# Optimization experiments

Measured on AMD Instinct MI355X. Metric: run time of the kernel, lower is better.

The kernel has to match this reference:

```python
import math
import jax, jax.numpy as jnp
import numpy as np

PROB_SPARSE_FACTOR = 0.4


def setup_inputs() -> dict:
    key = jax.random.key(0)
    kq, kk, kv = jax.random.split(key, 3)
    B, H, T, S, D = 2, 16, 2048, 2048, 64
    q = jax.random.normal(kq, (B, H, T, D), dtype=jnp.float32)
    k = jax.random.normal(kk, (B, H, S, D), dtype=jnp.float32)
    v = jax.random.normal(kv, (B, H, S, D), dtype=jnp.float32)
    return {"q": q, "k": k, "v": v}


def reference(q, k, v):
    B, H, T, D = q.shape
    S = k.shape[2]
    scaling = 1.0 / math.sqrt(D)
    # Informer-style top-u query count (static, derived from shapes)
    u = max(int(min(PROB_SPARSE_FACTOR * math.log(S), T * 0.5)), int(T * 0.3))

    # KLD scoring over full attention approximation: [B,H,T,S]
    attn_approx = jnp.einsum("bhtd,bhsd->bhts", q * scaling, k)
    attn_approx = jnp.clip(attn_approx, -50.0, 50.0)
    attn_approx = attn_approx - jnp.max(attn_approx, axis=-1, keepdims=True)
    sm = jax.nn.softmax(attn_approx, axis=-1)
    log_uniform = math.log(S)
    kl_score = jnp.sum(sm * (jnp.log(sm + 1e-10) + log_uniform), axis=-1)  # [B,H,T]

    # Select top-u most informative queries per (b,h)
    _, topk_idx = jax.lax.top_k(kl_score, u)  # [B,H,u]

    # Sparse attention only for selected queries
    q_red = jnp.take_along_axis(q, topk_idx[..., None], axis=2)  # [B,H,u,D]
    scores = jnp.einsum("bhud,bhsd->bhus", q_red, k) * scaling
    scores = jnp.clip(scores, -50.0, 50.0)
    scores = scores - jnp.max(scores, axis=-1, keepdims=True)
    w = jax.nn.softmax(scores, axis=-1)
    w = jnp.clip(w, 1e-9, 1.0)
    out_red = jnp.einsum("bhus,bhsd->bhud", w, v)  # [B,H,u,D]

    # Scatter reduced outputs back into a zero-initialized full output
    b_i = jnp.arange(B)[:, None, None]
    h_i = jnp.arange(H)[None, :, None]
    out = jnp.zeros_like(q).at[b_i, h_i, topk_idx].set(out_red)
    return out
```

## Files before the change

kernel.cpp:

```cpp
#include <hip/hip_runtime.h>
#include <math.h>

#define T_DIM 2048
#define S_DIM 2048
#define D_DIM 64
#define BH_DIM 32
#define U_SEL 614
#define QROWS 32
#define LOG_S_D 7.624618986159398
#define LOG2E_F 1.4426950408889634f
#define LN2_D 0.6931471805599453
#define SCL_Q (0.125f * LOG2E_F)

typedef __attribute__((ext_vector_type(8))) short bf16x8;
typedef __attribute__((ext_vector_type(4))) short bf16x4;
typedef __attribute__((ext_vector_type(4))) float f32x4;

__device__ __forceinline__ unsigned short bf16_rne(float x) {
  unsigned u = __float_as_uint(x);
  u += 0x7FFF + ((u >> 16) & 1);
  return (unsigned short)(u >> 16);
}
__device__ __forceinline__ float bf16_to_f(unsigned short h) {
  return __uint_as_float(((unsigned)h) << 16);
}
#if defined(__has_builtin)
#if __has_builtin(__builtin_amdgcn_exp2f)
#define EXP2_HW(x) __builtin_amdgcn_exp2f(x)
#endif
#endif
#ifndef EXP2_HW
#define EXP2_HW(x) exp2f(x)
#endif

#define GLD_LDS16(g, l)                                                        \
  __builtin_amdgcn_global_load_lds(                                            \
      (const __attribute__((address_space(1))) unsigned int*)(const void*)(g), \
      (__attribute__((address_space(3))) unsigned int*)(void*)(l), 16, 0, 0)

__device__ __forceinline__ void stage_img16(const unsigned short* __restrict__ g,
                                            unsigned short* l, int lane, int w) {
#pragma unroll
  for (int it = 0; it < 4; ++it) {
    const int chunk = it * 4 + w;
    GLD_LDS16((const char*)g + chunk * 1024 + lane * 16, (char*)l + chunk * 1024);
  }
}
__device__ __forceinline__ void stage_img8(const unsigned short* __restrict__ g,
                                           unsigned short* l, int lane, int w) {
#pragma unroll
  for (int it = 0; it < 2; ++it) {
    const int chunk = it * 4 + w;
    GLD_LDS16((const char*)g + chunk * 1024 + lane * 16, (char*)l + chunk * 1024);
  }
}

__device__ __forceinline__ bf16x8 ldfrag_sw(const unsigned short* buf, int row, int chunk) {
  return *(const bf16x8*)(buf + (row << 6) + (((chunk) ^ (row & 7)) << 3));
}
__device__ __forceinline__ bf16x8 ldfrag_k128(const unsigned short* buf, int row, int chunk) {
  return *(const bf16x8*)(buf + ((row >> 6) << 12) + ((row & 63) << 6) +
                          (((chunk) ^ (row & 7)) << 3));
}

__global__ __launch_bounds__(256) void convert_kernel(
    const float* __restrict__ kin, const float* __restrict__ vin,
    const float* __restrict__ qin, unsigned short* __restrict__ kimg,
    unsigned short* __restrict__ vt_g, unsigned short* __restrict__ qimg,
    float* __restrict__ out) {
  __shared__ float vld[128][65];
  const int jb = blockIdx.x;
  const int tid = threadIdx.x;
  if (jb < 2048) {
    const bool isq = jb >= 1024;
    const int jj = jb & 1023;
    const int bh = jj >> 5, tl = jj & 31;
    const float* src = (isq ? qin : kin) + ((size_t)bh * 2048 + tl * 64) * 64;
    unsigned short* dst = (isq ? qimg : kimg) + (size_t)(bh * 32 + tl) * 8192;
    const float scl = isq ? SCL_Q : 1.0f;
#pragma unroll
    for (int g = 0; g < 2; ++g) {
      const int flat = g * 256 + tid;
      const int r = flat >> 3, c = flat & 7;
      const float4 f0 = *(const float4*)(src + r * 64 + c * 8);
      const float4 f1 = *(const float4*)(src + r * 64 + c * 8 + 4);
      const float xs[8] = {f0.x, f0.y, f0.z, f0.w, f1.x, f1.y, f1.z, f1.w};
      bf16x8 hv, lv;
#pragma unroll
      for (int j = 0; j < 8; ++j) {
        const float x = xs[j] * scl;
        const unsigned short h = bf16_rne(x);
        hv[j] = (short)h;
        lv[j] = (short)bf16_rne(x - bf16_to_f(h));
      }
      const int base = (r << 6) + ((c ^ (r & 7)) << 3);
      *(bf16x8*)(dst + base) = hv;
      *(bf16x8*)(dst + 4096 + base) = lv;
    }
  } else if (jb < 2560) {
    const int jv = jb - 2048;
    const int bh = jv >> 4, tl = jv & 15;
    const float* src = vin + ((size_t)bh * 2048 + tl * 128) * 64;
#pragma unroll
    for (int g = 0; g < 8; ++g) {
      const int f = g * 256 + tid;
      const int r = f >> 4, c4 = f & 15;
      const float4 x = *(const float4*)(src + r * 64 + c4 * 4);
      vld[r][c4 * 4 + 0] = x.x;
      vld[r][c4 * 4 + 1] = x.y;
      vld[r][c4 * 4 + 2] = x.z;
      vld[r][c4 * 4 + 3] = x.w;
    }
    __syncthreads();
    unsigned short* dst = vt_g + (size_t)(bh * 16 + tl) * 8192;
#pragma unroll
    for (int g = 0; g < 4; ++g) {
      const int oc = g * 256 + tid;
      const int w4 = oc >> 8, dt = (oc >> 6) & 3, qd = (oc >> 4) & 3, l = oc & 15;
      bf16x8 hv;
#pragma unroll
      for (int j = 0; j < 8; ++j)
        hv[j] = (short)bf16_rne(vld[w4 * 32 + qd * 8 + j][dt * 16 + l]);
      *(bf16x8*)(dst + oc * 8) = hv;
    }
  } else {
    float4* o4 = (float4*)out;
    const size_t b = (size_t)(jb - 2560);
#pragma unroll
    for (int g = 0; g < 8; ++g)
      o4[b * 2048 + g * 256 + tid] = make_float4(0.f, 0.f, 0.f, 0.f);
  }
}

__global__ __launch_bounds__(256, 2) void kl_score_mfma(
    const unsigned short* __restrict__ qimg, const unsigned short* __restrict__ kimg,
    float2* __restrict__ zw) {
  __shared__ __align__(16) unsigned short lbuf[2][8192];
  const int b = blockIdx.x;
  const int bh = b & 31;
  const int tt = (b >> 5) & 15;
  const int shalf = b >> 9;
  const int tid = threadIdx.x;
  const int lane = tid & 63, w = tid >> 6, quad = lane >> 4, l15 = lane & 15;
  const unsigned short* qb = qimg + (size_t)(bh * 32 + tt * 2) * 8192;
  const unsigned short* kb = kimg + (size_t)bh * (32 * 8192);
  const int tg0 = shalf * 16;

  stage_img16(qb, &lbuf[0][0], lane, w);
  stage_img16(qb + 8192, &lbuf[1][0], lane, w);
  __syncthreads();

  bf16x8 ah[2][2], al[2][2];
#pragma unroll
  for (int rt = 0; rt < 2; ++rt) {
    const int row = w * 32 + rt * 16 + l15;
    const unsigned short* lb = &lbuf[row >> 6][0];
    const int r64 = row & 63;
#pragma unroll
    for (int kc = 0; kc < 2; ++kc) {
      const int off = (r64 << 6) + (((kc * 4 + quad) ^ (r64 & 7)) << 3);
      ah[rt][kc] = *(const bf16x8*)(lb + off);
      al[rt][kc] = *(const bf16x8*)(lb + 4096 + off);
    }
  }
  __syncthreads();

  stage_img16(kb + (size_t)tg0 * 8192, &lbuf[0][0], lane, w);
  __syncthreads();

  float Zf[8], Wf[8];
#pragma unroll
  for (int i = 0; i < 8; ++i) { Zf[i] = 0.f; Wf[i] = 0.f; }

  for (int t = 0; t < 16; ++t) {
    if (t < 15)
      stage_img16(kb + (size_t)(tg0 + t + 1) * 8192, &lbuf[(t + 1) & 1][0], lane, w);
    const unsigned short* cb = &lbuf[t & 1][0];

    f32x4 acc[2][4];
#pragma unroll
    for (int rt = 0; rt < 2; ++rt)
#pragma unroll
      for (int ct = 0; ct < 4; ++ct) acc[rt][ct] = (f32x4){0.f, 0.f, 0.f, 0.f};

#pragma unroll
    for (int ct = 0; ct < 4; ++ct) {
      const int srow = ct * 16 + l15;
      const bf16x8 bh0 = ldfrag_sw(cb, srow, quad);
      const bf16x8 bl0 = ldfrag_sw(cb + 4096, srow, quad);
      const bf16x8 bh1 = ldfrag_sw(cb, srow, 4 + quad);
      const bf16x8 bl1 = ldfrag_sw(cb + 4096, srow, 4 + quad);
#pragma unroll
      for (int rt = 0; rt < 2; ++rt) {
        f32x4 c = acc[rt][ct];
        c = __builtin_amdgcn_mfma_f32_16x16x32_bf16(ah[rt][0], bh0, c, 0, 0, 0);
        c = __builtin_amdgcn_mfma_f32_16x16x32_bf16(al[rt][0], bh0, c, 0, 0, 0);
        c = __builtin_amdgcn_mfma_f32_16x16x32_bf16(ah[rt][0], bl0, c, 0, 0, 0);
        c = __builtin_amdgcn_mfma_f32_16x16x32_bf16(ah[rt][1], bh1, c, 0, 0, 0);
        c = __builtin_amdgcn_mfma_f32_16x16x32_bf16(al[rt][1], bh1, c, 0, 0, 0);
        c = __builtin_amdgcn_mfma_f32_16x16x32_bf16(ah[rt][1], bl1, c, 0, 0, 0);
        acc[rt][ct] = c;
      }
    }

#pragma unroll
    for (int rt = 0; rt < 2; ++rt)
#pragma unroll
      for (int r = 0; r < 4; ++r) {
        float zp = 0.f, wp = 0.f;
#pragma unroll
        for (int ct = 0; ct < 4; ++ct) {
          const float tv = acc[rt][ct][r];
          const float e = EXP2_HW(tv);
          zp += e;
          wp = fmaf(e, tv, wp);
        }
        Zf[rt * 4 + r] += zp;
        Wf[rt * 4 + r] += wp;
      }
    __syncthreads();
  }

#pragma unroll
  for (int i = 0; i < 8; ++i) {
    float Zt = Zf[i], Wt = Wf[i];
#pragma unroll
    for (int mask = 1; mask <= 8; mask <<= 1) {
      Zt += __shfl_xor(Zt, mask);
      Wt += __shfl_xor(Wt, mask);
    }
    if (l15 == 0) {
      const int row = tt * 128 + w * 32 + (i >> 2) * 16 + quad * 4 + (i & 3);
      zw[((size_t)shalf * 32 + bh) * 2048 + row] = make_float2(Zt, Wt);
    }
  }
}

__global__ __launch_bounds__(1024) void topk_kernel(const float2* __restrict__ zw,
                                                    int* __restrict__ topk) {
  __shared__ float sv[2048];
  __shared__ int si[2048];
  const int bh = blockIdx.x;
  const int tid = threadIdx.x;
  for (int i = tid; i < 2048; i += 1024) {
    const float2 a = zw[(size_t)bh * 2048 + i];
    const float2 c = zw[(size_t)(32 + bh) * 2048 + i];
    const double Z = (double)a.x + (double)c.x;
    const double W = (double)a.y + (double)c.y;
    sv[i] = (float)(LN2_D * (W / Z) - log(Z) + LOG_S_D);
    si[i] = i;
  }
  __syncthreads();
  for (int kk = 2; kk <= 2048; kk <<= 1) {
    for (int j = kk >> 1; j > 0; j >>= 1) {
      const int p = tid;
      const int i = ((p & ~(j - 1)) << 1) | (p & (j - 1));
      const int pr = i | j;
      const float v1 = sv[i], v2 = sv[pr];
      const int i1 = si[i], i2 = si[pr];
      const bool beforePI = (v2 > v1) || (v2 == v1 && i2 < i1);
      const bool dirDesc = ((i & kk) == 0);
      const bool doSwap = dirDesc ? beforePI : !beforePI;
      if (doSwap) { sv[i] = v2; sv[pr] = v1; si[i] = i2; si[pr] = i1; }
      __syncthreads();
    }
  }
  for (int i = tid; i < U_SEL; i += 1024) topk[bh * U_SEL + i] = si[i];
}

struct __align__(16) SmC {
  union {
    unsigned short kt[2][8192];
    struct { float obuf[QROWS * 64]; float zred[4][QROWS]; } o;
  } a;
  union { unsigned short qs[QROWS * 64]; unsigned short ps[4][QROWS * 40]; } c;
};

__global__ __launch_bounds__(256, 3) void sparse_attn_mfma(
    const float* __restrict__ q, const unsigned short* __restrict__ kimg,
    const unsigned short* __restrict__ vt_g, const int* __restrict__ topk,
    float* __restrict__ out) {
  __shared__ SmC sm;
  const int b = blockIdx.x;
  const int bh = b & 31;
  const int l0 = (b >> 5) * QROWS;
  const int tid = threadIdx.x;
  const int lane = tid & 63, w = tid >> 6, quad = lane >> 4, l15 = lane & 15;
  const float* qb = q + (size_t)bh * (2048 * 64);
  const unsigned short* kb = kimg + (size_t)bh * (32 * 8192);
  const unsigned short* vtb = vt_g + (size_t)bh * (16 * 8192);
  const int* tkb = topk + bh * U_SEL;

  {
    const int ch = tid;
    const int r = ch >> 3, c = ch & 7;
    const int l = l0 + r;
    const int row = (l < U_SEL) ? tkb[l] : tkb[0];
    const float4 f0 = *(const float4*)(qb + (size_t)row * 64 + c * 8);
    const float4 f1 = *(const float4*)(qb + (size_t)row * 64 + c * 8 + 4);
    const float xs[8] = {f0.x, f0.y, f0.z, f0.w, f1.x, f1.y, f1.z, f1.w};
    bf16x8 hv;
#pragma unroll
    for (int j = 0; j < 8; ++j) hv[j] = (short)bf16_rne(xs[j] * SCL_Q);
    *(bf16x8*)&sm.c.qs[(r << 6) + ((c ^ (r & 7)) << 3)] = hv;
  }
  stage_img8(kb, sm.a.kt[0], lane, w);
  stage_img8(kb + 8192, sm.a.kt[0] + 4096, lane, w);
  __syncthreads();

  bf16x8 qf[2][2];
#pragma unroll
  for (int nt = 0; nt < 2; ++nt)
#pragma unroll
    for (int kc = 0; kc < 2; ++kc)
      qf[nt][kc] = ldfrag_sw(sm.c.qs, nt * 16 + l15, kc * 4 + quad);
  __syncthreads();

  float zrun[2] = {0.f, 0.f};
  f32x4 oacc[2][4];
#pragma unroll
  for (int a = 0; a < 2; ++a)
#pragma unroll
    for (int b2 = 0; b2 < 4; ++b2) oacc[a][b2] = (f32x4){0.f, 0.f, 0.f, 0.f};

  for (int st = 0; st < 16; ++st) {
    if (st < 15) {
      unsigned short* kd = sm.a.kt[(st + 1) & 1];
      stage_img8(kb + (size_t)(2 * st + 2) * 8192, kd, lane, w);
      stage_img8(kb + (size_t)(2 * st + 3) * 8192, kd + 4096, lane, w);
    }
    const char* vp = (const char*)(vtb + (size_t)st * 8192);
    bf16x8 vbf[4];
#pragma unroll
    for (int dt = 0; dt < 4; ++dt)
      vbf[dt] = *(const bf16x8*)(vp + w * 4096 + dt * 1024 + lane * 16);

    const unsigned short* kcur = sm.a.kt[st & 1];

    const int ar0 = w * 32 + l15, ar1 = w * 32 + 16 + l15;
    const bf16x8 a00 = ldfrag_k128(kcur, ar0, quad);
    const bf16x8 a01 = ldfrag_k128(kcur, ar0, 4 + quad);
    const bf16x8 a10 = ldfrag_k128(kcur, ar1, quad);
    const bf16x8 a11 = ldfrag_k128(kcur, ar1, 4 + quad);

    f32x4 sacc[2][2];
    __builtin_amdgcn_s_setprio(1);
#pragma unroll
    for (int mt = 0; mt < 2; ++mt)
#pragma unroll
      for (int nt = 0; nt < 2; ++nt) {
        f32x4 c = (f32x4){0.f, 0.f, 0.f, 0.f};
        c = __builtin_amdgcn_mfma_f32_16x16x32_bf16(mt ? a10 : a00, qf[nt][0], c, 0, 0, 0);
        c = __builtin_amdgcn_mfma_f32_16x16x32_bf16(mt ? a11 : a01, qf[nt][1], c, 0, 0, 0);
        sacc[mt][nt] = c;
      }
    __builtin_amdgcn_s_setprio(0);

#pragma unroll
    for (int nt = 0; nt < 2; ++nt) {
      float zl = 0.f;
#pragma unroll
      for (int mt = 0; mt < 2; ++mt) {
        bf16x4 pw;
#pragma unroll
        for (int r = 0; r < 4; ++r) {
          const float p = EXP2_HW(sacc[mt][nt][r]);
          zl += p;
          pw[r] = (short)bf16_rne(p);
        }
        *(bf16x4*)&sm.c.ps[w][(nt * 16 + l15) * 40 + mt * 16 + quad * 4] = pw;
      }
      zrun[nt] += zl;
    }

    __builtin_amdgcn_s_setprio(1);
#pragma unroll
    for (int mtq = 0; mtq < 2; ++mtq) {
      const bf16x8 pa = *(const bf16x8*)&sm.c.ps[w][(mtq * 16 + l15) * 40 + quad * 8];
#pragma unroll
      for (int dt = 0; dt < 4; ++dt)
        oacc[mtq][dt] = __builtin_amdgcn_mfma_f32_16x16x32_bf16(pa, vbf[dt], oacc[mtq][dt], 0, 0, 0);
    }
    __builtin_amdgcn_s_setprio(0);
    __syncthreads();
  }

#pragma unroll
  for (int nt = 0; nt < 2; ++nt) {
    float z = zrun[nt];
    z += __shfl_xor(z, 16);
    z += __shfl_xor(z, 32);
    if (quad == 0) sm.a.o.zred[w][nt * 16 + l15] = z;
  }
  for (int i = tid; i < QROWS * 64; i += 256) sm.a.o.obuf[i] = 0.f;
  __syncthreads();
#pragma unroll
  for (int mtq = 0; mtq < 2; ++mtq)
#pragma unroll
    for (int r = 0; r < 4; ++r) {
      const int qr = mtq * 16 + quad * 4 + r;
#pragma unroll
      for (int dt = 0; dt < 4; ++dt)
        atomicAdd(&sm.a.o.obuf[qr * 64 + dt * 16 + l15], oacc[mtq][dt][r]);
    }
  __syncthreads();
  {
    if (tid < QROWS * 4) {
      const int qr = tid >> 2, seg = tid & 3;
      const int l = l0 + qr;
      if (l < U_SEL) {
        const float Zt = sm.a.o.zred[0][qr] + sm.a.o.zred[1][qr] +
                         sm.a.o.zred[2][qr] + sm.a.o.zred[3][qr];
        const float inv = 1.0f / Zt;
        const int row = tkb[l];
        float* op = &out[((size_t)bh * T_DIM + row) * 64 + seg * 16];
        const float* ob = &sm.a.o.obuf[qr * 64 + seg * 16];
#pragma unroll
        for (int j = 0; j < 4; ++j) {
          float4 o;
          o.x = ob[j * 4 + 0] * inv;
          o.y = ob[j * 4 + 1] * inv;
          o.z = ob[j * 4 + 2] * inv;
          o.w = ob[j * 4 + 3] * inv;
          *(float4*)&op[j * 4] = o;
        }
      }
    }
  }
}

extern "C" void kernel_launch(void* const* d_in, const int* in_sizes, int n_in,
                              void* d_out, int out_size, void* d_ws, size_t ws_size,
                              hipStream_t stream) {
  const float* q = (const float*)d_in[0];
  const float* k = (const float*)d_in[1];
  const float* v = (const float*)d_in[2];
  float* out = (float*)d_out;
  char* ws = (char*)d_ws;
  float2* zw = (float2*)ws;
  int* topk = (int*)(ws + 1048576);
  unsigned short* kimg = (unsigned short*)(ws + 1310720);
  unsigned short* vt_g = (unsigned short*)(ws + 18087936);
  unsigned short* qimg = (unsigned short*)(ws + 26476544);

  convert_kernel<<<dim3(3072), dim3(256), 0, stream>>>(k, v, q, kimg, vt_g, qimg, out);
  kl_score_mfma<<<dim3(1024), dim3(256), 0, stream>>>(qimg, kimg, zw);
  topk_kernel<<<dim3(BH_DIM), dim3(1024), 0, stream>>>(zw, topk);
  sparse_attn_mfma<<<dim3(768), dim3(256), 0, stream>>>(q, kimg, vt_g, topk, out);
}
```

Measured before the change: 220.2 us.

## Pre-layout K in MFMA fragment order and load directly to registers

The convert kernel now also writes a third copy of the high bf16 part of K, laid out in MFMA fragment order per wave. The sparse attention kernel loads its A fragments straight from global memory into registers, so the LDS double-buffered K staging and the per-iteration __syncthreads are gone. This lowers LDS use and removes block-wide barriers in the main loop. In exchange the convert kernel does extra global writes, and global load latency is no longer hidden by the asynchronous LDS prefetch.

```diff
diff --git a/kernel.cpp b/kernel.cpp
--- a/kernel.cpp
+++ b/kernel.cpp
@@ -46,14 +46,6 @@
     GLD_LDS16((const char*)g + chunk * 1024 + lane * 16, (char*)l + chunk * 1024);
   }
 }
-__device__ __forceinline__ void stage_img8(const unsigned short* __restrict__ g,
-                                           unsigned short* l, int lane, int w) {
-#pragma unroll
-  for (int it = 0; it < 2; ++it) {
-    const int chunk = it * 4 + w;
-    GLD_LDS16((const char*)g + chunk * 1024 + lane * 16, (char*)l + chunk * 1024);
-  }
-}
 
 __device__ __forceinline__ bf16x8 ldfrag_sw(const unsigned short* buf, int row, int chunk) {
   return *(const bf16x8*)(buf + (row << 6) + (((chunk) ^ (row & 7)) << 3));
@@ -67,7 +59,7 @@
     const float* __restrict__ kin, const float* __restrict__ vin,
     const float* __restrict__ qin, unsigned short* __restrict__ kimg,
     unsigned short* __restrict__ vt_g, unsigned short* __restrict__ qimg,
-    float* __restrict__ out) {
+    unsigned short* __restrict__ kcimg, float* __restrict__ out) {
   __shared__ float vld[128][65];
   const int jb = blockIdx.x;
   const int tid = threadIdx.x;
@@ -77,6 +69,7 @@
     const int bh = jj >> 5, tl = jj & 31;
     const float* src = (isq ? qin : kin) + ((size_t)bh * 2048 + tl * 64) * 64;
     unsigned short* dst = (isq ? qimg : kimg) + (size_t)(bh * 32 + tl) * 8192;
+    unsigned short* kcd = kcimg + (size_t)(bh * 16 + (tl >> 1)) * 8192;
     const float scl = isq ? SCL_Q : 1.0f;
 #pragma unroll
     for (int g = 0; g < 2; ++g) {
@@ -96,6 +89,11 @@
       const int base = (r << 6) + ((c ^ (r & 7)) << 3);
       *(bf16x8*)(dst + base) = hv;
       *(bf16x8*)(dst + 4096 + base) = lv;
+      if (!isq) {
+        const int s_local = ((tl & 1) << 6) + r;
+        const int wv = s_local >> 5, mtk = (r >> 4) & 1, kcc = c >> 2, qdd = c & 3;
+        *(bf16x8*)(kcd + (wv * 4 + mtk * 2 + kcc) * 512 + qdd * 128 + ((r & 15) << 3)) = hv;
+      }
     }
   } else if (jb < 2560) {
     const int jv = jb - 2048;
@@ -269,15 +267,13 @@
 }
 
 struct __align__(16) SmC {
-  union {
-    unsigned short kt[2][8192];
-    struct { float obuf[QROWS * 64]; float zred[4][QROWS]; } o;
-  } a;
   union { unsigned short qs[QROWS * 64]; unsigned short ps[4][QROWS * 40]; } c;
+  float obuf[QROWS * 64];
+  float zred[4][QROWS];
 };
 
 __global__ __launch_bounds__(256, 3) void sparse_attn_mfma(
-    const float* __restrict__ q, const unsigned short* __restrict__ kimg,
+    const float* __restrict__ q, const unsigned short* __restrict__ kcimg,
     const unsigned short* __restrict__ vt_g, const int* __restrict__ topk,
     float* __restrict__ out) {
   __shared__ SmC sm;
@@ -287,13 +283,12 @@
   const int tid = threadIdx.x;
   const int lane = tid & 63, w = tid >> 6, quad = lane >> 4, l15 = lane & 15;
   const float* qb = q + (size_t)bh * (2048 * 64);
-  const unsigned short* kb = kimg + (size_t)bh * (32 * 8192);
-  const unsigned short* vtb = vt_g + (size_t)bh * (16 * 8192);
+  const char* kcb = (const char*)(kcimg + (size_t)bh * (16 * 8192));
+  const char* vtb = (const char*)(vt_g + (size_t)bh * (16 * 8192));
   const int* tkb = topk + bh * U_SEL;
 
   {
-    const int ch = tid;
-    const int r = ch >> 3, c = ch & 7;
+    const int r = tid >> 3, c = tid & 7;
     const int l = l0 + r;
     const int row = (l < U_SEL) ? tkb[l] : tkb[0];
     const float4 f0 = *(const float4*)(qb + (size_t)row * 64 + c * 8);
@@ -304,8 +299,6 @@
     for (int j = 0; j < 8; ++j) hv[j] = (short)bf16_rne(xs[j] * SCL_Q);
     *(bf16x8*)&sm.c.qs[(r << 6) + ((c ^ (r & 7)) << 3)] = hv;
   }
-  stage_img8(kb, sm.a.kt[0], lane, w);
-  stage_img8(kb + 8192, sm.a.kt[0] + 4096, lane, w);
   __syncthreads();
 
   bf16x8 qf[2][2];
@@ -324,24 +317,18 @@
     for (int b2 = 0; b2 < 4; ++b2) oacc[a][b2] = (f32x4){0.f, 0.f, 0.f, 0.f};
 
   for (int st = 0; st < 16; ++st) {
-    if (st < 15) {
-      unsigned short* kd = sm.a.kt[(st + 1) & 1];
-      stage_img8(kb + (size_t)(2 * st + 2) * 8192, kd, lane, w);
-      stage_img8(kb + (size_t)(2 * st + 3) * 8192, kd + 4096, lane, w);
-    }
-    const char* vp = (const char*)(vtb + (size_t)st * 8192);
+    const char* kp = kcb + (size_t)st * 16384;
+    bf16x8 af[2][2];
+#pragma unroll
+    for (int mt = 0; mt < 2; ++mt)
+#pragma unroll
+      for (int kc = 0; kc < 2; ++kc)
+        af[mt][kc] = *(const bf16x8*)(kp + ((w * 4 + mt * 2 + kc) << 10) + lane * 16);
+    const char* vp = vtb + (size_t)st * 16384;
     bf16x8 vbf[4];
 #pragma unroll
     for (int dt = 0; dt < 4; ++dt)
-      vbf[dt] = *(const bf16x8*)(vp + w * 4096 + dt * 1024 + lane * 16);
-
-    const unsigned short* kcur = sm.a.kt[st & 1];
-
-    const int ar0 = w * 32 + l15, ar1 = w * 32 + 16 + l15;
-    const bf16x8 a00 = ldfrag_k128(kcur, ar0, quad);
-    const bf16x8 a01 = ldfrag_k128(kcur, ar0, 4 + quad);
-    const bf16x8 a10 = ldfrag_k128(kcur, ar1, quad);
-    const bf16x8 a11 = ldfrag_k128(kcur, ar1, 4 + quad);
+      vbf[dt] = *(const bf16x8*)(vp + ((w * 4 + dt) << 10) + lane * 16);
 
     f32x4 sacc[2][2];
     __builtin_amdgcn_s_setprio(1);
@@ -350,8 +337,8 @@
 #pragma unroll
       for (int nt = 0; nt < 2; ++nt) {
         f32x4 c = (f32x4){0.f, 0.f, 0.f, 0.f};
-        c = __builtin_amdgcn_mfma_f32_16x16x32_bf16(mt ? a10 : a00, qf[nt][0], c, 0, 0, 0);
-        c = __builtin_amdgcn_mfma_f32_16x16x32_bf16(mt ? a11 : a01, qf[nt][1], c, 0, 0, 0);
+        c = __builtin_amdgcn_mfma_f32_16x16x32_bf16(af[mt][0], qf[nt][0], c, 0, 0, 0);
+        c = __builtin_amdgcn_mfma_f32_16x16x32_bf16(af[mt][1], qf[nt][1], c, 0, 0, 0);
         sacc[mt][nt] = c;
       }
     __builtin_amdgcn_s_setprio(0);
@@ -382,7 +369,6 @@
         oacc[mtq][dt] = __builtin_amdgcn_mfma_f32_16x16x32_bf16(pa, vbf[dt], oacc[mtq][dt], 0, 0, 0);
     }
     __builtin_amdgcn_s_setprio(0);
-    __syncthreads();
   }
 
 #pragma unroll
@@ -390,9 +376,9 @@
     float z = zrun[nt];
     z += __shfl_xor(z, 16);
     z += __shfl_xor(z, 32);
-    if (quad == 0) sm.a.o.zred[w][nt * 16 + l15] = z;
-  }
-  for (int i = tid; i < QROWS * 64; i += 256) sm.a.o.obuf[i] = 0.f;
+    if (quad == 0) sm.zred[w][nt * 16 + l15] = z;
+  }
+  for (int i = tid; i < QROWS * 64; i += 256) sm.obuf[i] = 0.f;
   __syncthreads();
 #pragma unroll
   for (int mtq = 0; mtq < 2; ++mtq)
@@ -401,7 +387,7 @@
       const int qr = mtq * 16 + quad * 4 + r;
 #pragma unroll
       for (int dt = 0; dt < 4; ++dt)
-        atomicAdd(&sm.a.o.obuf[qr * 64 + dt * 16 + l15], oacc[mtq][dt][r]);
+        atomicAdd(&sm.obuf[qr * 64 + dt * 16 + l15], oacc[mtq][dt][r]);
     }
   __syncthreads();
   {
@@ -409,12 +395,12 @@
       const int qr = tid >> 2, seg = tid & 3;
       const int l = l0 + qr;
       if (l < U_SEL) {
-        const float Zt = sm.a.o.zred[0][qr] + sm.a.o.zred[1][qr] +
-                         sm.a.o.zred[2][qr] + sm.a.o.zred[3][qr];
+        const float Zt = sm.zred[0][qr] + sm.zred[1][qr] +
+                         sm.zred[2][qr] + sm.zred[3][qr];
         const float inv = 1.0f / Zt;
         const int row = tkb[l];
         float* op = &out[((size_t)bh * T_DIM + row) * 64 + seg * 16];
-        const float* ob = &sm.a.o.obuf[qr * 64 + seg * 16];
+        const float* ob = &sm.obuf[qr * 64 + seg * 16];
 #pragma unroll
         for (int j = 0; j < 4; ++j) {
           float4 o;
@@ -442,9 +428,10 @@
   unsigned short* kimg = (unsigned short*)(ws + 1310720);
   unsigned short* vt_g = (unsigned short*)(ws + 18087936);
   unsigned short* qimg = (unsigned short*)(ws + 26476544);
-
-  convert_kernel<<<dim3(3072), dim3(256), 0, stream>>>(k, v, q, kimg, vt_g, qimg, out);
+  unsigned short* kcimg = (unsigned short*)(ws + 43253760);
+
+  convert_kernel<<<dim3(3072), dim3(256), 0, stream>>>(k, v, q, kimg, vt_g, qimg, kcimg, out);
   kl_score_mfma<<<dim3(1024), dim3(256), 0, stream>>>(qimg, kimg, zw);
   topk_kernel<<<dim3(BH_DIM), dim3(1024), 0, stream>>>(zw, topk);
-  sparse_attn_mfma<<<dim3(768), dim3(256), 0, stream>>>(q, kimg, vt_g, topk, out);
-}
+  sparse_attn_mfma<<<dim3(768), dim3(256), 0, stream>>>(q, kcimg, vt_g, topk, out);
+}
```

Result: no change. 221.6 us (+0.6%).
